# Kernel tuning notes

Hardware: AMD Instinct MI355X
Metric: run time of the kernel (lower is better)

The kernel has to match this reference:

```python
import jax, jax.numpy as jnp
import numpy as np

OS = 14            # output_size
GRID = 2           # ceil(roi_size/OS) = ceil(28/14) = 2 (boxes are built 28x28, sampling_ratio=-1)
NODES = OS * OS    # 196 graph nodes
EPS = 1e-5         # BatchNorm eps
K, B, C, H, W = 256, 4, 256, 112, 112


def _bn_relu(x, g, b, m, v):
    # eval-mode BatchNorm2d followed by ReLU (bn_act_conv prefix)
    s = jax.lax.rsqrt(v + EPS)
    xn = (x - m[None, :, None, None]) * s[None, :, None, None]
    return jax.nn.relu(xn * g[None, :, None, None] + b[None, :, None, None])


def _conv(x, w, b, pad):
    y = jax.lax.conv_general_dilated(x, w, (1, 1), [(pad, pad), (pad, pad)],
                                     dimension_numbers=('NCHW', 'OIHW', 'NCHW'))
    return y + b[None, :, None, None]


def _roi_align(sem, boxes):
    # torchvision roi_align, spatial_scale=1.0, aligned=False, sampling_ratio=-1 (static grid=2)
    Bs, Cc, Hh, Ww = sem.shape
    bidx = boxes[:, 0].astype(jnp.int32)
    x1, y1, x2, y2 = boxes[:, 1], boxes[:, 2], boxes[:, 3], boxes[:, 4]
    bw = jnp.maximum(x2 - x1, 1.0) / OS
    bh = jnp.maximum(y2 - y1, 1.0) / OS
    t = (jnp.arange(OS * GRID, dtype=sem.dtype) + 0.5) / GRID   # pw*GRID+ix collapsed
    xs = x1[:, None] + bw[:, None] * t                          # [K, 28]
    ys = y1[:, None] + bh[:, None] * t

    def prep(c, L):
        m = (c >= -1.0) & (c <= L)
        cc = jnp.clip(c, 0.0, L - 1)
        lo = jnp.floor(cc).astype(jnp.int32)
        hi = jnp.minimum(lo + 1, L - 1)
        return m, lo, hi, cc - lo

    my, yl, yh, ly = prep(ys, Hh)
    mx, xl, xh, lx = prep(xs, Ww)
    semt = jnp.transpose(sem, (0, 2, 3, 1))  # [B,H,W,C]

    def gat(ya, xa):
        return semt[bidx[:, None, None], ya[:, :, None], xa[:, None, :]]  # [K,28,28,C]

    ly_ = ly[:, :, None, None]
    lx_ = lx[:, None, :, None]
    val = (gat(yl, xl) * (1 - ly_) * (1 - lx_) + gat(yl, xh) * (1 - ly_) * lx_
           + gat(yh, xl) * ly_ * (1 - lx_) + gat(yh, xh) * ly_ * lx_)
    val = jnp.where((my[:, :, None] & mx[:, None, :])[..., None], val, 0.0)
    val = val.reshape(-1, OS, GRID, OS, GRID, Cc).mean(axis=(2, 4))  # avg over sampling grid
    return jnp.transpose(val, (0, 3, 1, 2))  # [K,C,14,14]


def _gcn_agg(A, x):
    # PyG gcn_norm on a fully-connected weighted graph (self loops already present):
    # deg[j] = sum_i A[i,j] (scatter on col); out[j] = sum_i d^-1/2[i] A[i,j] d^-1/2[j] x[i]
    deg = A.sum(axis=1)                 # [K,196]
    dis = jax.lax.rsqrt(deg)            # sigmoid weights > 0 => no zero degree
    Nrm = dis[:, :, None] * A * dis[:, None, :]
    return jnp.einsum('kij,kif->kjf', Nrm, x)


def _forward(roi_feature, semantic, boxes,
             bn_sem_g, bn_sem_b, bn_sem_m, bn_sem_v, conv_sem_w, conv_sem_b,
             bn_fpn_g, bn_fpn_b, bn_fpn_m, bn_fpn_v, conv_fpn_w, conv_fpn_b,
             bn_aff_g, bn_aff_b, bn_aff_m, bn_aff_v, conv_aff_w, conv_aff_b,
             gcn1_w, gcn1_b, gcn2_w, gcn2_b):
    roi_sem = _roi_align(semantic, boxes)                                   # [K,256,14,14]
    a = (_conv(_bn_relu(roi_sem, bn_sem_g, bn_sem_b, bn_sem_m, bn_sem_v), conv_sem_w, conv_sem_b, 1)
         + _conv(_bn_relu(roi_feature, bn_fpn_g, bn_fpn_b, bn_fpn_m, bn_fpn_v), conv_fpn_w, conv_fpn_b, 1))
    aff = _conv(_bn_relu(a, bn_aff_g, bn_aff_b, bn_aff_m, bn_aff_v), conv_aff_w, conv_aff_b, 0)
    A = jax.nn.sigmoid(aff.reshape(-1, NODES, NODES))                       # [K,196,196]
    X = roi_feature.reshape(-1, C, NODES).transpose(0, 2, 1)                # [K,196,256] node feats
    x1 = jax.nn.relu(_gcn_agg(A, X @ gcn1_w) + gcn1_b)                      # GCNConv(256,16)+ReLU
    x2 = _gcn_agg(A, x1 @ gcn2_w) + gcn2_b                                  # GCNConv(16,256)
    emb = x2.transpose(0, 2, 1).reshape(-1, C, OS, OS)
    return roi_sem + emb


def setup_inputs() -> dict:
    key = jax.random.key(0)
    ks = jax.random.split(key, 24)
    roi_feature = jax.random.normal(ks[0], (K, C, OS, OS), jnp.float32)
    semantic = jax.random.normal(ks[1], (B, C, H, W), jnp.float32)
    bidx = jax.random.randint(ks[2], (K,), 0, B).astype(jnp.float32)
    xy = jax.random.uniform(ks[3], (K, 2), jnp.float32, 0.0, float(H - 28))
    boxes = jnp.concatenate([bidx[:, None], xy, xy + 28.0], axis=1)  # (idx,x1,y1,x2,y2), 28x28 boxes

    def bn(kg, c):
        k1, k2, k3, k4 = jax.random.split(kg, 4)
        return (jax.random.normal(k1, (c,)) * 0.1 + 1.0,
                jax.random.normal(k2, (c,)) * 0.1,
                jax.random.normal(k3, (c,)) * 0.1,
                jax.random.uniform(k4, (c,), jnp.float32, 0.5, 1.5))
    bn_sem = bn(ks[4], C); bn_fpn = bn(ks[5], C); bn_aff = bn(ks[6], 64)
    inp = {
        'roi_feature': roi_feature, 'semantic': semantic, 'boxes': boxes,
        'bn_sem_g': bn_sem[0], 'bn_sem_b': bn_sem[1], 'bn_sem_m': bn_sem[2], 'bn_sem_v': bn_sem[3],
        'conv_sem_w': jax.random.normal(ks[7], (64, C, 3, 3)) * 0.02,
        'conv_sem_b': jax.random.normal(ks[8], (64,)) * 0.02,
        'bn_fpn_g': bn_fpn[0], 'bn_fpn_b': bn_fpn[1], 'bn_fpn_m': bn_fpn[2], 'bn_fpn_v': bn_fpn[3],
        'conv_fpn_w': jax.random.normal(ks[9], (64, C, 3, 3)) * 0.02,
        'conv_fpn_b': jax.random.normal(ks[10], (64,)) * 0.02,
        'bn_aff_g': bn_aff[0], 'bn_aff_b': bn_aff[1], 'bn_aff_m': bn_aff[2], 'bn_aff_v': bn_aff[3],
        'conv_aff_w': jax.random.normal(ks[11], (NODES, 64, 1, 1)) * 0.05,
        'conv_aff_b': jax.random.normal(ks[12], (NODES,)) * 0.05,
        'gcn1_w': jax.random.normal(ks[13], (C, 16)) * 0.05,
        'gcn1_b': jax.random.normal(ks[14], (16,)) * 0.05,
        'gcn2_w': jax.random.normal(ks[15], (16, C)) * 0.05,
        'gcn2_b': jax.random.normal(ks[16], (C,)) * 0.05,
    }
    return inp


def reference(roi_feature, semantic, boxes,
              bn_sem_g, bn_sem_b, bn_sem_m, bn_sem_v, conv_sem_w, conv_sem_b,
              bn_fpn_g, bn_fpn_b, bn_fpn_m, bn_fpn_v, conv_fpn_w, conv_fpn_b,
              bn_aff_g, bn_aff_b, bn_aff_m, bn_aff_v, conv_aff_w, conv_aff_b,
              gcn1_w, gcn1_b, gcn2_w, gcn2_b):
    return _forward(roi_feature, semantic, boxes,
                    bn_sem_g, bn_sem_b, bn_sem_m, bn_sem_v, conv_sem_w, conv_sem_b,
                    bn_fpn_g, bn_fpn_b, bn_fpn_m, bn_fpn_v, conv_fpn_w, conv_fpn_b,
                    bn_aff_g, bn_aff_b, bn_aff_m, bn_aff_v, conv_aff_w, conv_aff_b,
                    gcn1_w, gcn1_b, gcn2_w, gcn2_b)
```

## Files before the change

### kernel.cpp

```cpp
#include <hip/hip_runtime.h>
#include <hip/hip_bf16.h>

#define KBOX 256
#define CCH  256
#define NODES 196
#define OS 14

typedef __attribute__((ext_vector_type(8))) short  bf16x8;
typedef __attribute__((ext_vector_type(8))) unsigned short u16x8;
typedef __attribute__((ext_vector_type(4))) float  f32x4;
typedef __attribute__((ext_vector_type(4))) short  s16x4;
typedef __attribute__((ext_vector_type(4))) int    i32x4;

__device__ __forceinline__ short f2bf(float x) {
  __hip_bfloat16 h = __float2bfloat16(x);
  return *reinterpret_cast<short*>(&h);
}
__device__ __forceinline__ float bf2f(unsigned short u) {
  unsigned int x = ((unsigned int)u) << 16;
  union { unsigned int i; float f; } c; c.i = x;
  return c.f;
}

#define MFMA16 __builtin_amdgcn_mfma_f32_16x16x32_bf16

__global__ __launch_bounds__(256) void prep_kernel(
    const float* __restrict__ bn_sem_g, const float* __restrict__ bn_sem_b,
    const float* __restrict__ bn_sem_m, const float* __restrict__ bn_sem_v,
    const float* __restrict__ conv_sem_w, const float* __restrict__ conv_sem_b,
    const float* __restrict__ bn_fpn_g, const float* __restrict__ bn_fpn_b,
    const float* __restrict__ bn_fpn_m, const float* __restrict__ bn_fpn_v,
    const float* __restrict__ conv_fpn_w, const float* __restrict__ conv_fpn_b,
    const float* __restrict__ bn_aff_g, const float* __restrict__ bn_aff_b,
    const float* __restrict__ bn_aff_m, const float* __restrict__ bn_aff_v,
    const float* __restrict__ conv_aff_w, const float* __restrict__ g1w,
    const float* __restrict__ g2w,
    float* __restrict__ ss_sem, float* __restrict__ ss_fpn, float* __restrict__ ss_aff2,
    short* __restrict__ wfrag, short* __restrict__ wafrag, short* __restrict__ g1wf,
    short* __restrict__ g2wf)
{
  int gid = blockIdx.x * blockDim.x + threadIdx.x;
  int gsz = gridDim.x * blockDim.x;
  for (int c = gid; c < 256; c += gsz) {
    float s = bn_sem_g[c] * rsqrtf(bn_sem_v[c] + 1e-5f);
    ss_sem[c] = s; ss_sem[256 + c] = bn_sem_b[c] - bn_sem_m[c] * s;
    float s2 = bn_fpn_g[c] * rsqrtf(bn_fpn_v[c] + 1e-5f);
    ss_fpn[c] = s2; ss_fpn[256 + c] = bn_fpn_b[c] - bn_fpn_m[c] * s2;
  }
  for (int c = gid; c < 64; c += gsz) {
    float s = bn_aff_g[c] * rsqrtf(bn_aff_v[c] + 1e-5f);
    float sh = bn_aff_b[c] - bn_aff_m[c] * s;
    float bias = conv_sem_b[c] + conv_fpn_b[c];
    ss_aff2[c] = s; ss_aff2[64 + c] = bias * s + sh;
  }
  for (int idx = gid; idx < 144 * 4 * 64 * 8; idx += gsz) {
    int e = idx & 7, lane = (idx >> 3) & 63, nt = (idx >> 9) & 3, kstep = idx >> 11;
    int src = kstep / 72, rem = kstep % 72, icc = rem / 9, pos = rem % 9;
    int ky = pos / 3, kx = pos % 3;
    int oc = nt * 16 + (lane & 15);
    int ic = icc * 32 + (lane >> 4) * 8 + e;
    const float* w = src ? conv_fpn_w : conv_sem_w;
    wfrag[idx] = f2bf(w[((oc * 256 + ic) * 3 + ky) * 3 + kx]);
  }
  for (int idx = gid; idx < 2 * 13 * 64 * 8; idx += gsz) {
    int t = idx;
    int e = t & 7; t >>= 3;
    int lane = t & 63; t >>= 6;
    int nt = t % 13; int s = t / 13;
    int i = nt * 16 + (lane & 15);
    int ic = s * 32 + (lane >> 4) * 8 + e;
    wafrag[idx] = f2bf(i < NODES ? conv_aff_w[i * 64 + ic] : 0.f);
  }
  for (int idx = gid; idx < 8 * 64 * 8; idx += gsz) {
    int e = idx & 7, lane = (idx >> 3) & 63, ks = idx >> 9;
    int ic = ks * 32 + (lane >> 4) * 8 + e;
    int f = lane & 15;
    g1wf[idx] = f2bf(g1w[ic * 16 + f]);
  }
  for (int idx = gid; idx < 16 * 64 * 8; idx += gsz) {
    int e = idx & 7, lane = (idx >> 3) & 63, ct = idx >> 9;
    int kk = (lane >> 4) * 8 + e;
    int c = ct * 16 + (lane & 15);
    g2wf[idx] = f2bf(kk < 16 ? g2w[kk * 256 + c] : 0.f);
  }
}

__global__ __launch_bounds__(256) void transpose_bf16_kernel(
    const float* __restrict__ in, unsigned short* __restrict__ out, int C, int HW)
{
  __shared__ float tile[64][65];
  int nh = (HW + 63) >> 6;
  int bi = blockIdx.x;
  int cb = bi % (C >> 6); bi /= (C >> 6);
  int hb = bi % nh; int b = bi / nh;
  int tx = threadIdx.x & 63, ty = threadIdx.x >> 6;
  const float* inb = in + (size_t)b * C * HW;
  unsigned short* outb = out + (size_t)b * HW * C;
  #pragma unroll
  for (int i = ty; i < 64; i += 4) {
    int c = cb * 64 + i, hw = hb * 64 + tx;
    tile[i][tx] = (hw < HW) ? inb[(size_t)c * HW + hw] : 0.f;
  }
  __syncthreads();
  int cp = threadIdx.x & 31;
  #pragma unroll
  for (int i = (int)(threadIdx.x >> 5); i < 64; i += 8) {
    int hw = hb * 64 + i;
    if (hw < HW) {
      ushort2 v;
      v.x = (unsigned short)f2bf(tile[cp * 2][i]);
      v.y = (unsigned short)f2bf(tile[cp * 2 + 1][i]);
      *(ushort2*)&outb[(size_t)hw * C + cb * 64 + cp * 2] = v;
    }
  }
}

__global__ __launch_bounds__(512) void roi_align_kernel(
    const unsigned short* __restrict__ semt, const float* __restrict__ boxes,
    unsigned short* __restrict__ roi_sem)
{
  __shared__ unsigned short slab[5][29][256];
  int kb = blockIdx.x / 7, g = blockIdx.x % 7;
  int tid = threadIdx.x, wave = tid >> 6, lane = tid & 63;
  const float* bx = boxes + kb * 5;
  int bb = (int)bx[0];
  float x1 = bx[1], y1 = bx[2];
  float xb = x1 + 0.5f, yv = y1 + 0.5f;
  int X0 = (int)floorf(xb); float fx = xb - (float)X0;
  int Y0 = (int)floorf(yv); float fy = yv - (float)Y0;
  const unsigned short* base = semt + (size_t)bb * 12544 * 256;
  #pragma unroll
  for (int i = 0; i < 19; ++i) {
    int s = wave + i * 8;
    if (s < 145) {
      int r = s / 29, xi = s - r * 29;
      int yr = min(Y0 + 4 * g + r, 111);
      int xc = min(X0 + xi, 111);
      *(s16x4*)&slab[r][xi][lane * 4] =
          *(const s16x4*)(base + ((size_t)yr * 112 + xc) * 256 + lane * 4);
    }
  }
  __syncthreads();
  int c2 = tid & 127, grp = tid >> 7;
  int oyl = grp >> 1, og = grp & 1;
  int rb = oyl * 2;
  float w0 = 1.f - fy;
  unsigned short* op = roi_sem + (((size_t)kb * NODES) + (2 * g + oyl) * OS) * 256 + c2 * 2;
  #pragma unroll
  for (int oxs = 0; oxs < 7; ++oxs) {
    int ox = og * 7 + oxs;
    float o0 = 0.f, o1 = 0.f;
    #pragma unroll
    for (int xi = 0; xi < 3; ++xi) {
      float xw = (xi == 0) ? (1.f - fx) : (xi == 1 ? 1.f : fx);
      const unsigned short* p0 = &slab[rb][2 * ox + xi][c2 * 2];
      const unsigned short* p1 = &slab[rb + 1][2 * ox + xi][c2 * 2];
      const unsigned short* p2 = &slab[rb + 2][2 * ox + xi][c2 * 2];
      o0 += xw * (w0 * bf2f(p0[0]) + bf2f(p1[0]) + fy * bf2f(p2[0]));
      o1 += xw * (w0 * bf2f(p0[1]) + bf2f(p1[1]) + fy * bf2f(p2[1]));
    }
    ushort2 v;
    v.x = (unsigned short)f2bf(o0 * 0.25f);
    v.y = (unsigned short)f2bf(o1 * 0.25f);
    *(ushort2*)(op + (size_t)ox * 256) = v;
  }
}

__global__ __launch_bounds__(256) void conv_ab_kernel(
    const unsigned short* __restrict__ roi_sem, const unsigned short* __restrict__ roif,
    const float* __restrict__ ss_sem, const float* __restrict__ ss_fpn,
    const short* __restrict__ wfrag, const float* __restrict__ ss_aff2,
    short* __restrict__ a_rel)
{
  int k = blockIdx.x;
  int tid = threadIdx.x;
  int wave = tid >> 6, lane = tid & 63;
  int l15 = lane & 15, lq = lane >> 4;
  __shared__ short lds_in[2][197][40];
  __shared__ short lds_wf[2][18432];
  __shared__ float lds_sc[2][256], lds_sh[2][256];
  __shared__ float scA[64], cmbA[64];

  lds_sc[0][tid] = ss_sem[tid]; lds_sh[0][tid] = ss_sem[256 + tid];
  lds_sc[1][tid] = ss_fpn[tid]; lds_sh[1][tid] = ss_fpn[256 + tid];
  if (tid < 64) { scA[tid] = ss_aff2[tid]; cmbA[tid] = ss_aff2[64 + tid]; }
  if (tid < 40) { lds_in[0][196][tid] = 0; lds_in[1][196][tid] = 0; }

  int oyA[4], oxA[4]; bool mvA[4], jvA[4];
  #pragma unroll
  for (int mi = 0; mi < 4; ++mi) {
    int mt = wave + mi * 4;
    mvA[mi] = (mt < 13);
    int j = mt * 16 + l15;
    jvA[mi] = (j < 196);
    int oy = j / 14;
    oyA[mi] = oy; oxA[mi] = j - oy * 14;
  }

  u16x8 inv[4];
  i32x4 wv[9];
  const size_t kbase = (size_t)k * NODES * CCH;

  f32x4 acc[4][4];
  #pragma unroll
  for (int i = 0; i < 4; ++i)
    #pragma unroll
    for (int j = 0; j < 4; ++j) acc[i][j] = f32x4{0.f, 0.f, 0.f, 0.f};

#define ISSUE_LOADS(P) do {                                                  \
    int src_ = (P) >> 3, icc_ = (P) & 7;                                     \
    const unsigned short* in_ = (src_ ? roif : roi_sem) + kbase + icc_ * 32; \
    _Pragma("unroll")                                                        \
    for (int i_ = 0; i_ < 3; ++i_) {                                         \
      int f_ = tid + i_ * 256;                                               \
      inv[i_] = *(const u16x8*)(in_ + (size_t)(f_ >> 2) * 256 + (f_ & 3) * 8); \
    }                                                                        \
    if (tid < 16) {                                                          \
      int f_ = 768 + tid;                                                    \
      inv[3] = *(const u16x8*)(in_ + (size_t)(f_ >> 2) * 256 + (f_ & 3) * 8); \
    }                                                                        \
    const i32x4* wsl_ = (const i32x4*)(wfrag + (size_t)(src_ * 72 + icc_ * 9) * 2048); \
    _Pragma("unroll")                                                        \
    for (int i_ = 0; i_ < 9; ++i_) wv[i_] = wsl_[tid + i_ * 256];            \
  } while (0)

#define WRITE_STAGE(P, BUF) do {                                             \
    int src_ = (P) >> 3, icc_ = (P) & 7;                                     \
    _Pragma("unroll")                                                        \
    for (int i_ = 0; i_ < 3; ++i_) {                                         \
      int f_ = tid + i_ * 256;                                               \
      int j_ = f_ >> 2, cq_ = f_ & 3;                                        \
      bf16x8 pk_;                                                            \
      _Pragma("unroll")                                                      \
      for (int u_ = 0; u_ < 8; ++u_) {                                       \
        int c_ = icc_ * 32 + cq_ * 8 + u_;                                   \
        float x_ = bf2f(inv[i_][u_]) * lds_sc[src_][c_] + lds_sh[src_][c_];  \
        pk_[u_] = f2bf(fmaxf(x_, 0.f));                                      \
      }                                                                      \
      *(bf16x8*)&lds_in[BUF][j_][cq_ * 8] = pk_;                             \
    }                                                                        \
    if (tid < 16) {                                                          \
      int f_ = 768 + tid; int j_ = f_ >> 2, cq_ = f_ & 3;                    \
      bf16x8 pk_;                                                            \
      _Pragma("unroll")                                                      \
      for (int u_ = 0; u_ < 8; ++u_) {                                       \
        int c_ = icc_ * 32 + cq_ * 8 + u_;                                   \
        float x_ = bf2f(inv[3][u_]) * lds_sc[src_][c_] + lds_sh[src_][c_];   \
        pk_[u_] = f2bf(fmaxf(x_, 0.f));                                      \
      }                                                                      \
      *(bf16x8*)&lds_in[BUF][j_][cq_ * 8] = pk_;                             \
    }                                                                        \
    _Pragma("unroll")                                                        \
    for (int i_ = 0; i_ < 9; ++i_) ((i32x4*)lds_wf[BUF])[tid + i_ * 256] = wv[i_]; \
  } while (0)

  ISSUE_LOADS(0);
  __syncthreads();
  WRITE_STAGE(0, 0);
  ISSUE_LOADS(1);
  __syncthreads();

  for (int p = 0; p < 16; ++p) {
    int buf = p & 1;
    if (p < 15) WRITE_STAGE(p + 1, buf ^ 1);
    if (p < 14) ISSUE_LOADS(p + 2);
    #pragma unroll
    for (int pos = 0; pos < 9; ++pos) {
      int ky = pos / 3 - 1, kx = pos % 3 - 1;
      bf16x8 bfr[4];
      #pragma unroll
      for (int n = 0; n < 4; ++n)
        bfr[n] = *(const bf16x8*)&lds_wf[buf][((pos * 4 + n) * 64 + lane) * 8];
      #pragma unroll
      for (int mi = 0; mi < 4; ++mi) {
        if (!mvA[mi]) continue;
        int ny = oyA[mi] + ky, nx = oxA[mi] + kx;
        bool v = jvA[mi] & ((unsigned)ny < 14u) & ((unsigned)nx < 14u);
        int np = v ? (ny * 14 + nx) : 196;
        bf16x8 afr = *(const bf16x8*)&lds_in[buf][np][lq * 8];
        acc[mi][0] = MFMA16(afr, bfr[0], acc[mi][0], 0, 0, 0);
        acc[mi][1] = MFMA16(afr, bfr[1], acc[mi][1], 0, 0, 0);
        acc[mi][2] = MFMA16(afr, bfr[2], acc[mi][2], 0, 0, 0);
        acc[mi][3] = MFMA16(afr, bfr[3], acc[mi][3], 0, 0, 0);
      }
    }
    __syncthreads();
  }

  #pragma unroll
  for (int mi = 0; mi < 4; ++mi) {
    int mt = wave + mi * 4;
    if (mt >= 13) continue;
    #pragma unroll
    for (int n = 0; n < 4; ++n) {
      int oc = n * 16 + l15;
      float sa = scA[oc], cb = cmbA[oc];
      #pragma unroll
      for (int r = 0; r < 4; ++r) {
        int j = mt * 16 + lq * 4 + r;
        if (j < NODES) {
          float t = fmaxf(acc[mi][n][r] * sa + cb, 0.f);
          a_rel[((size_t)k * NODES + j) * 64 + oc] = f2bf(t);
        }
      }
    }
  }
#undef ISSUE_LOADS
#undef WRITE_STAGE
}

__global__ __launch_bounds__(1024, 1) void graph_kernel(
    const short* __restrict__ a_rel, const short* __restrict__ wafrag,
    const float* __restrict__ aff_b, const short* __restrict__ g1wf,
    const float* __restrict__ g1b, const unsigned short* __restrict__ roif_bf,
    const short* __restrict__ g2wf, const float* __restrict__ g2b,
    const unsigned short* __restrict__ roi_sem, float* __restrict__ outp)
{
  __shared__ __align__(16) char smem[125840];
  const int tid = threadIdx.x, wave = tid >> 6, lane = tid & 63;
  const int l15 = lane & 15, lq = lane >> 4;
  const int k = blockIdx.x;

  char*  Ab   = smem;
  short* wa   = (short*)(smem + 96512);
  short* yfr  = (short*)(smem + 96512);
  short* zsf  = (short*)(smem + 103680);
  float* dsl  = (float*)(smem + 123136);
  float* g1bl = (float*)(smem + 123968);
  float* g2bl = (float*)(smem + 124032);
  float* affb = (float*)(smem + 125056);

  const bool wv13 = (wave < 13);
  const int jr  = wave * 16 + l15;
  const int jrc = min(jr, 195);
  const i32x4 z4 = {};

  bf16x8 af0 = {}, af1 = {};
  if (wv13) {
    const short* ap = a_rel + (size_t)k * 12544 + jrc * 64 + lq * 8;
    af0 = *(const bf16x8*)ap;
    af1 = *(const bf16x8*)(ap + 32);
  }
  {
    i32x4 w0 = ((const i32x4*)wafrag)[tid];
    i32x4 w1 = z4;
    if (tid < 640) w1 = ((const i32x4*)wafrag)[1024 + tid];
    if (tid < 832) {
      int r = tid >> 2, q = tid & 3;
      *(i32x4*)(Ab + r * 464 + 384 + q * 16) = z4;
    }
    if (tid < 196) affb[tid] = aff_b[tid];
    if (tid < 256) g2bl[tid] = g2b[tid];
    if (tid < 16)  g1bl[tid] = g1b[tid];
    ((i32x4*)wa)[tid] = w0;
    if (tid < 640) ((i32x4*)wa)[1024 + tid] = w1;
  }
  __syncthreads();

  if (wv13) {
    float rsum[4] = {0.f, 0.f, 0.f, 0.f};
    #pragma unroll
    for (int n = 0; n < 13; ++n) {
      bf16x8 b0 = *(const bf16x8*)(wa + (n * 64 + lane) * 8);
      bf16x8 b1 = *(const bf16x8*)(wa + ((13 + n) * 64 + lane) * 8);
      f32x4 acc = {0.f, 0.f, 0.f, 0.f};
      acc = MFMA16(af0, b0, acc, 0, 0, 0);
      acc = MFMA16(af1, b1, acc, 0, 0, 0);
      int i = n * 16 + l15;
      bool iv = (i < 196);
      float bv = affb[iv ? i : 0];
      #pragma unroll
      for (int r = 0; r < 4; ++r) {
        float v = acc[r] + bv;
        float s = 1.f / (1.f + __expf(-v));
        if (iv) {
          rsum[r] += s;
          *(short*)(Ab + (wave * 16 + lq * 4 + r) * 464 + i * 2) = f2bf(s);
        }
      }
    }
    #pragma unroll
    for (int r = 0; r < 4; ++r) {
      float v = rsum[r];
      v += __shfl_xor(v, 1); v += __shfl_xor(v, 2);
      v += __shfl_xor(v, 4); v += __shfl_xor(v, 8);
      int j = wave * 16 + lq * 4 + r;
      if (l15 == 0 && j < 196) dsl[j] = rsqrtf(v);
    }
  }
  __syncthreads();

  *(i32x4*)(smem + 96512 + tid * 16) = z4;
  if (tid < 256) *(i32x4*)(smem + 96512 + (1024 + tid) * 16) = z4;
  f32x4 xacc = {0.f, 0.f, 0.f, 0.f};
  if (wv13) {
    const unsigned short* Xp = roif_bf + (size_t)k * 50176 + (size_t)jrc * 256 + lq * 8;
    #pragma unroll
    for (int ks = 0; ks < 8; ++ks) {
      bf16x8 xa = *(const bf16x8*)(Xp + ks * 32);
      bf16x8 xb = *(const bf16x8*)(g1wf + (ks * 64 + lane) * 8);
      xacc = MFMA16(xa, xb, xacc, 0, 0, 0);
    }
  }
  __syncthreads();

  if (wv13) {
    #pragma unroll
    for (int r = 0; r < 4; ++r) {
      int i = wave * 16 + lq * 4 + r;
      if (i < 196) {
        float yv = dsl[i] * xacc[r];
        yfr[((i >> 5) * 64 + ((i >> 3) & 3) * 16 + l15) * 8 + (i & 7)] = f2bf(yv);
      }
    }
  }
  __syncthreads();

  f32x4 g0 = {0.f, 0.f, 0.f, 0.f};
  if (wv13) {
    #pragma unroll
    for (int ks = 0; ks < 7; ++ks) {
      bf16x8 bb = *(const bf16x8*)(yfr + (ks * 64 + lane) * 8);
      bf16x8 a0 = *(const bf16x8*)(Ab + jr * 464 + ks * 64 + lq * 16);
      g0 = MFMA16(a0, bb, g0, 0, 0, 0);
    }
  }
  __syncthreads();
  if (wv13) {
    #pragma unroll
    for (int r = 0; r < 4; ++r) {
      int i = wave * 16 + lq * 4 + r;
      if (i < 196) {
        float d = dsl[i];
        float x1v = fmaxf(g0[r] * d + g1bl[l15], 0.f);
        yfr[((i >> 5) * 64 + ((i >> 3) & 3) * 16 + l15) * 8 + (i & 7)] = f2bf(d * x1v);
      }
    }
  }
  __syncthreads();

  if (wv13) {
    f32x4 z0 = {0.f, 0.f, 0.f, 0.f};
    #pragma unroll
    for (int ks = 0; ks < 7; ++ks) {
      bf16x8 bb = *(const bf16x8*)(yfr + (ks * 64 + lane) * 8);
      bf16x8 a0 = *(const bf16x8*)(Ab + jr * 464 + ks * 64 + lq * 16);
      z0 = MFMA16(a0, bb, z0, 0, 0, 0);
    }
    #pragma unroll
    for (int r = 0; r < 4; ++r) {
      int j = wave * 16 + lq * 4 + r;
      if (j < 196) {
        float zv = z0[r] * dsl[j];
        zsf[((j >> 4) * 64 + (l15 >> 3) * 16 + (j & 15)) * 8 + (l15 & 7)] = f2bf(zv);
      }
    }
  }
  __syncthreads();

  {
    bf16x8 wf = *(const bf16x8*)(g2wf + (wave * 64 + lane) * 8);
    const unsigned short* rsmk = roi_sem + (size_t)k * 50176;
    float* op = outp + (size_t)k * 50176;
    float gbv[4];
    #pragma unroll
    for (int r = 0; r < 4; ++r) gbv[r] = g2bl[wave * 16 + lq * 4 + r];
    #pragma unroll
    for (int jt = 0; jt < 13; ++jt) {
      bf16x8 zb = *(const bf16x8*)(zsf + (jt * 64 + lane) * 8);
      f32x4 d = {0.f, 0.f, 0.f, 0.f};
      d = MFMA16(wf, zb, d, 0, 0, 0);
      int j = jt * 16 + l15;
      if (j < 196) {
        #pragma unroll
        for (int r = 0; r < 4; ++r) {
          int c = wave * 16 + lq * 4 + r;
          op[(size_t)c * 196 + j] = d[r] + gbv[r] + bf2f(rsmk[(size_t)j * 256 + c]);
        }
      }
    }
  }
}

extern "C" void kernel_launch(void* const* d_in, const int* in_sizes, int n_in,
                              void* d_out, int out_size, void* d_ws, size_t ws_size,
                              hipStream_t stream) {
  const float* roi_feature = (const float*)d_in[0];
  const float* semantic    = (const float*)d_in[1];
  const float* boxes       = (const float*)d_in[2];
  const float* bn_sem_g = (const float*)d_in[3];
  const float* bn_sem_b = (const float*)d_in[4];
  const float* bn_sem_m = (const float*)d_in[5];
  const float* bn_sem_v = (const float*)d_in[6];
  const float* conv_sem_w = (const float*)d_in[7];
  const float* conv_sem_b = (const float*)d_in[8];
  const float* bn_fpn_g = (const float*)d_in[9];
  const float* bn_fpn_b = (const float*)d_in[10];
  const float* bn_fpn_m = (const float*)d_in[11];
  const float* bn_fpn_v = (const float*)d_in[12];
  const float* conv_fpn_w = (const float*)d_in[13];
  const float* conv_fpn_b = (const float*)d_in[14];
  const float* bn_aff_g = (const float*)d_in[15];
  const float* bn_aff_b = (const float*)d_in[16];
  const float* bn_aff_m = (const float*)d_in[17];
  const float* bn_aff_v = (const float*)d_in[18];
  const float* conv_aff_w = (const float*)d_in[19];
  const float* conv_aff_b = (const float*)d_in[20];
  const float* gcn1_w = (const float*)d_in[21];
  const float* gcn1_b = (const float*)d_in[22];
  const float* gcn2_w = (const float*)d_in[23];
  const float* gcn2_b = (const float*)d_in[24];

  const size_t FT = (size_t)KBOX * NODES * CCH;
  unsigned short* ws16      = (unsigned short*)d_ws;
  unsigned short* semt_bf   = ws16;
  unsigned short* roif_bf   = semt_bf + FT;
  unsigned short* roi_sem_b = roif_bf + FT;
  short*          a_rel     = (short*)(roi_sem_b + FT);
  float*          ss_sem    = (float*)(a_rel + 3211264);
  float*          ss_fpn    = ss_sem + 512;
  float*          ss_aff2   = ss_fpn + 512;
  short*          wfrag     = (short*)(ss_aff2 + 128);
  short*          wafrag    = wfrag + 294912;
  short*          g1wf      = wafrag + 13312;
  short*          g2wf      = g1wf + 4096;

  prep_kernel<<<256, 256, 0, stream>>>(
      bn_sem_g, bn_sem_b, bn_sem_m, bn_sem_v, conv_sem_w, conv_sem_b,
      bn_fpn_g, bn_fpn_b, bn_fpn_m, bn_fpn_v, conv_fpn_w, conv_fpn_b,
      bn_aff_g, bn_aff_b, bn_aff_m, bn_aff_v, conv_aff_w, gcn1_w, gcn2_w,
      ss_sem, ss_fpn, ss_aff2, wfrag, wafrag, g1wf, g2wf);

  transpose_bf16_kernel<<<4 * 196 * 4, 256, 0, stream>>>(semantic, semt_bf, 256, 12544);
  transpose_bf16_kernel<<<4 * 4 * 256, 256, 0, stream>>>(roi_feature, roif_bf, 256, 196);
  roi_align_kernel<<<KBOX * 7, 512, 0, stream>>>(semt_bf, boxes, roi_sem_b);
  conv_ab_kernel<<<KBOX, 256, 0, stream>>>(roi_sem_b, roif_bf, ss_sem, ss_fpn, wfrag, ss_aff2, a_rel);
  graph_kernel<<<KBOX, 1024, 0, stream>>>(a_rel, wafrag, conv_aff_b, g1wf, gcn1_b, roif_bf,
                                          g2wf, gcn2_b, roi_sem_b, (float*)d_out);
}
```

Measured before the change: 161.5 us.

## Split conv over kernel positions across 8 waves with LDS reduction

Rewrites the fused 3x3 conv kernel to use 512 threads. Each wave pair takes a subset of the 9 kernel taps and half the output channels. Each block stages all 256 input channels of one source into LDS at once, padded to a row stride of 268, instead of double-buffering 32-channel slices. Weight fragments are now read straight from global memory rather than through LDS. Partial sums from the tap groups are combined through an LDS reduction before the BN/ReLU epilogue. This adds more parallel waves per block and removes the per-slice pipeline syncs, at the cost of 104 accumulator registers per lane, uneven tap counts across groups, and global weight reads inside the MFMA loop.

```diff
diff --git a/kernel.cpp b/kernel.cpp
--- a/kernel.cpp
+++ b/kernel.cpp
@@ -166,147 +166,160 @@
   }
 }
 
-__global__ __launch_bounds__(256) void conv_ab_kernel(
+__global__ __launch_bounds__(512) void conv_ab_kernel(
     const unsigned short* __restrict__ roi_sem, const unsigned short* __restrict__ roif,
     const float* __restrict__ ss_sem, const float* __restrict__ ss_fpn,
-    const short* __restrict__ wfrag, const float* __restrict__ ss_aff2,
+    const float* __restrict__ ss_aff2, const short* __restrict__ wfrag,
     short* __restrict__ a_rel)
 {
-  int k = blockIdx.x;
-  int tid = threadIdx.x;
-  int wave = tid >> 6, lane = tid & 63;
-  int l15 = lane & 15, lq = lane >> 4;
-  __shared__ short lds_in[2][197][40];
-  __shared__ short lds_wf[2][18432];
-  __shared__ float lds_sc[2][256], lds_sh[2][256];
+  __shared__ short inLDS[198 * 268];
   __shared__ float scA[64], cmbA[64];
-
-  lds_sc[0][tid] = ss_sem[tid]; lds_sh[0][tid] = ss_sem[256 + tid];
-  lds_sc[1][tid] = ss_fpn[tid]; lds_sh[1][tid] = ss_fpn[256 + tid];
+  const int k = blockIdx.x;
+  const int tid = threadIdx.x;
+  const int wave = tid >> 6, lane = tid & 63;
+  const int l15 = lane & 15, lq = lane >> 4;
+  const int pg = wave >> 1, ng = wave & 1;
+  const int p0 = (pg == 0) ? 0 : (pg * 2 + 1);
+  const int p1 = p0 + ((pg == 0) ? 3 : 2);
+
   if (tid < 64) { scA[tid] = ss_aff2[tid]; cmbA[tid] = ss_aff2[64 + tid]; }
-  if (tid < 40) { lds_in[0][196][tid] = 0; lds_in[1][196][tid] = 0; }
-
-  int oyA[4], oxA[4]; bool mvA[4], jvA[4];
+  if (tid < 34) {
+    bf16x8 z = {};
+    *(bf16x8*)&inLDS[196 * 268 + tid * 8] = z;
+  }
+
+  int oyA[13], oxA[13];
   #pragma unroll
-  for (int mi = 0; mi < 4; ++mi) {
-    int mt = wave + mi * 4;
-    mvA[mi] = (mt < 13);
+  for (int mt = 0; mt < 13; ++mt) {
     int j = mt * 16 + l15;
-    jvA[mi] = (j < 196);
     int oy = j / 14;
-    oyA[mi] = oy; oxA[mi] = j - oy * 14;
-  }
-
-  u16x8 inv[4];
-  i32x4 wv[9];
-  const size_t kbase = (size_t)k * NODES * CCH;
-
-  f32x4 acc[4][4];
+    oyA[mt] = oy; oxA[mt] = j - oy * 14;
+  }
+  const int c0 = (tid & 31) * 8;
+
+  f32x4 acc[13][2];
   #pragma unroll
-  for (int i = 0; i < 4; ++i)
-    #pragma unroll
-    for (int j = 0; j < 4; ++j) acc[i][j] = f32x4{0.f, 0.f, 0.f, 0.f};
-
-#define ISSUE_LOADS(P) do {                                                  \
-    int src_ = (P) >> 3, icc_ = (P) & 7;                                     \
-    const unsigned short* in_ = (src_ ? roif : roi_sem) + kbase + icc_ * 32; \
-    _Pragma("unroll")                                                        \
-    for (int i_ = 0; i_ < 3; ++i_) {                                         \
-      int f_ = tid + i_ * 256;                                               \
-      inv[i_] = *(const u16x8*)(in_ + (size_t)(f_ >> 2) * 256 + (f_ & 3) * 8); \
-    }                                                                        \
-    if (tid < 16) {                                                          \
-      int f_ = 768 + tid;                                                    \
-      inv[3] = *(const u16x8*)(in_ + (size_t)(f_ >> 2) * 256 + (f_ & 3) * 8); \
-    }                                                                        \
-    const i32x4* wsl_ = (const i32x4*)(wfrag + (size_t)(src_ * 72 + icc_ * 9) * 2048); \
-    _Pragma("unroll")                                                        \
-    for (int i_ = 0; i_ < 9; ++i_) wv[i_] = wsl_[tid + i_ * 256];            \
-  } while (0)
-
-#define WRITE_STAGE(P, BUF) do {                                             \
-    int src_ = (P) >> 3, icc_ = (P) & 7;                                     \
-    _Pragma("unroll")                                                        \
-    for (int i_ = 0; i_ < 3; ++i_) {                                         \
-      int f_ = tid + i_ * 256;                                               \
-      int j_ = f_ >> 2, cq_ = f_ & 3;                                        \
-      bf16x8 pk_;                                                            \
-      _Pragma("unroll")                                                      \
-      for (int u_ = 0; u_ < 8; ++u_) {                                       \
-        int c_ = icc_ * 32 + cq_ * 8 + u_;                                   \
-        float x_ = bf2f(inv[i_][u_]) * lds_sc[src_][c_] + lds_sh[src_][c_];  \
-        pk_[u_] = f2bf(fmaxf(x_, 0.f));                                      \
-      }                                                                      \
-      *(bf16x8*)&lds_in[BUF][j_][cq_ * 8] = pk_;                             \
-    }                                                                        \
-    if (tid < 16) {                                                          \
-      int f_ = 768 + tid; int j_ = f_ >> 2, cq_ = f_ & 3;                    \
-      bf16x8 pk_;                                                            \
-      _Pragma("unroll")                                                      \
-      for (int u_ = 0; u_ < 8; ++u_) {                                       \
-        int c_ = icc_ * 32 + cq_ * 8 + u_;                                   \
-        float x_ = bf2f(inv[3][u_]) * lds_sc[src_][c_] + lds_sh[src_][c_];   \
-        pk_[u_] = f2bf(fmaxf(x_, 0.f));                                      \
-      }                                                                      \
-      *(bf16x8*)&lds_in[BUF][j_][cq_ * 8] = pk_;                             \
-    }                                                                        \
-    _Pragma("unroll")                                                        \
-    for (int i_ = 0; i_ < 9; ++i_) ((i32x4*)lds_wf[BUF])[tid + i_ * 256] = wv[i_]; \
-  } while (0)
-
-  ISSUE_LOADS(0);
-  __syncthreads();
-  WRITE_STAGE(0, 0);
-  ISSUE_LOADS(1);
-  __syncthreads();
-
-  for (int p = 0; p < 16; ++p) {
-    int buf = p & 1;
-    if (p < 15) WRITE_STAGE(p + 1, buf ^ 1);
-    if (p < 14) ISSUE_LOADS(p + 2);
-    #pragma unroll
-    for (int pos = 0; pos < 9; ++pos) {
+  for (int mt = 0; mt < 13; ++mt) {
+    acc[mt][0] = f32x4{0.f, 0.f, 0.f, 0.f};
+    acc[mt][1] = f32x4{0.f, 0.f, 0.f, 0.f};
+  }
+
+  for (int src = 0; src < 2; ++src) {
+    const unsigned short* inp = (src ? roif : roi_sem) + (size_t)k * NODES * CCH;
+    const float* ss = src ? ss_fpn : ss_sem;
+    f32x4 sc0 = *(const f32x4*)(ss + c0);
+    f32x4 sc1 = *(const f32x4*)(ss + c0 + 4);
+    f32x4 sh0 = *(const f32x4*)(ss + 256 + c0);
+    f32x4 sh1 = *(const f32x4*)(ss + 256 + c0 + 4);
+    __syncthreads();
+    #pragma unroll
+    for (int i = 0; i < 12; ++i) {
+      int j = (tid >> 5) + i * 16;
+      u16x8 v = *(const u16x8*)(inp + (size_t)j * 256 + c0);
+      bf16x8 pk;
+      #pragma unroll
+      for (int u = 0; u < 4; ++u) pk[u] = f2bf(fmaxf(bf2f(v[u]) * sc0[u] + sh0[u], 0.f));
+      #pragma unroll
+      for (int u = 0; u < 4; ++u) pk[4 + u] = f2bf(fmaxf(bf2f(v[4 + u]) * sc1[u] + sh1[u], 0.f));
+      *(bf16x8*)&inLDS[j * 268 + c0] = pk;
+    }
+    if (tid < 128) {
+      int j = 192 + (tid >> 5);
+      u16x8 v = *(const u16x8*)(inp + (size_t)j * 256 + c0);
+      bf16x8 pk;
+      #pragma unroll
+      for (int u = 0; u < 4; ++u) pk[u] = f2bf(fmaxf(bf2f(v[u]) * sc0[u] + sh0[u], 0.f));
+      #pragma unroll
+      for (int u = 0; u < 4; ++u) pk[4 + u] = f2bf(fmaxf(bf2f(v[4 + u]) * sc1[u] + sh1[u], 0.f));
+      *(bf16x8*)&inLDS[j * 268 + c0] = pk;
+    }
+    __syncthreads();
+
+    for (int pos = p0; pos < p1; ++pos) {
       int ky = pos / 3 - 1, kx = pos % 3 - 1;
-      bf16x8 bfr[4];
-      #pragma unroll
-      for (int n = 0; n < 4; ++n)
-        bfr[n] = *(const bf16x8*)&lds_wf[buf][((pos * 4 + n) * 64 + lane) * 8];
-      #pragma unroll
-      for (int mi = 0; mi < 4; ++mi) {
-        if (!mvA[mi]) continue;
-        int ny = oyA[mi] + ky, nx = oxA[mi] + kx;
-        bool v = jvA[mi] & ((unsigned)ny < 14u) & ((unsigned)nx < 14u);
-        int np = v ? (ny * 14 + nx) : 196;
-        bf16x8 afr = *(const bf16x8*)&lds_in[buf][np][lq * 8];
-        acc[mi][0] = MFMA16(afr, bfr[0], acc[mi][0], 0, 0, 0);
-        acc[mi][1] = MFMA16(afr, bfr[1], acc[mi][1], 0, 0, 0);
-        acc[mi][2] = MFMA16(afr, bfr[2], acc[mi][2], 0, 0, 0);
-        acc[mi][3] = MFMA16(afr, bfr[3], acc[mi][3], 0, 0, 0);
-      }
-    }
-    __syncthreads();
-  }
-
-  #pragma unroll
-  for (int mi = 0; mi < 4; ++mi) {
-    int mt = wave + mi * 4;
-    if (mt >= 13) continue;
-    #pragma unroll
-    for (int n = 0; n < 4; ++n) {
-      int oc = n * 16 + l15;
-      float sa = scA[oc], cb = cmbA[oc];
-      #pragma unroll
-      for (int r = 0; r < 4; ++r) {
-        int j = mt * 16 + lq * 4 + r;
-        if (j < NODES) {
-          float t = fmaxf(acc[mi][n][r] * sa + cb, 0.f);
-          a_rel[((size_t)k * NODES + j) * 64 + oc] = f2bf(t);
-        }
-      }
-    }
-  }
-#undef ISSUE_LOADS
-#undef WRITE_STAGE
+      int np[13];
+      #pragma unroll
+      for (int mt = 0; mt < 13; ++mt) {
+        int ny = oyA[mt] + ky, nx = oxA[mt] + kx;
+        bool v = ((unsigned)ny < 14u) & ((unsigned)nx < 14u) & ((mt * 16 + l15) < 196);
+        np[mt] = v ? (ny * 14 + nx) : 196;
+      }
+      #pragma unroll
+      for (int icc = 0; icc < 8; ++icc) {
+        const short* wp = wfrag +
+            ((size_t)((src * 72 + icc * 9 + pos) * 4 + ng * 2) * 64 + lane) * 8;
+        bf16x8 b0 = *(const bf16x8*)wp;
+        bf16x8 b1 = *(const bf16x8*)(wp + 512);
+        #pragma unroll
+        for (int mt = 0; mt < 13; ++mt) {
+          bf16x8 a = *(const bf16x8*)&inLDS[np[mt] * 268 + icc * 32 + lq * 8];
+          acc[mt][0] = MFMA16(a, b0, acc[mt][0], 0, 0, 0);
+          acc[mt][1] = MFMA16(a, b1, acc[mt][1], 0, 0, 0);
+        }
+      }
+    }
+  }
+
+  float* red = (float*)inLDS;
+  __syncthreads();
+  if (pg == 1 || pg == 3) {
+    float* dst = red + (size_t)((pg >> 1) * 2 + ng) * 6272;
+    #pragma unroll
+    for (int mt = 0; mt < 13; ++mt)
+      #pragma unroll
+      for (int nn = 0; nn < 2; ++nn)
+        #pragma unroll
+        for (int r = 0; r < 4; ++r) {
+          int j = mt * 16 + lq * 4 + r;
+          if (j < 196) dst[j * 32 + nn * 16 + l15] = acc[mt][nn][r];
+        }
+  }
+  __syncthreads();
+  if (pg == 0 || pg == 2) {
+    const float* sb = red + (size_t)((pg >> 1) * 2 + ng) * 6272;
+    #pragma unroll
+    for (int mt = 0; mt < 13; ++mt)
+      #pragma unroll
+      for (int nn = 0; nn < 2; ++nn)
+        #pragma unroll
+        for (int r = 0; r < 4; ++r) {
+          int j = mt * 16 + lq * 4 + r;
+          if (j < 196) acc[mt][nn][r] += sb[j * 32 + nn * 16 + l15];
+        }
+  }
+  __syncthreads();
+  if (pg == 2) {
+    float* dst = red + (size_t)ng * 6272;
+    #pragma unroll
+    for (int mt = 0; mt < 13; ++mt)
+      #pragma unroll
+      for (int nn = 0; nn < 2; ++nn)
+        #pragma unroll
+        for (int r = 0; r < 4; ++r) {
+          int j = mt * 16 + lq * 4 + r;
+          if (j < 196) dst[j * 32 + nn * 16 + l15] = acc[mt][nn][r];
+        }
+  }
+  __syncthreads();
+  if (pg == 0) {
+    const float* sb = red + (size_t)ng * 6272;
+    short* op = a_rel + (size_t)k * 12544;
+    #pragma unroll
+    for (int mt = 0; mt < 13; ++mt)
+      #pragma unroll
+      for (int nn = 0; nn < 2; ++nn) {
+        int oc = (ng * 2 + nn) * 16 + l15;
+        float sa = scA[oc], cb = cmbA[oc];
+        #pragma unroll
+        for (int r = 0; r < 4; ++r) {
+          int j = mt * 16 + lq * 4 + r;
+          if (j < 196) {
+            float t = acc[mt][nn][r] + sb[j * 32 + nn * 16 + l15];
+            op[j * 64 + oc] = f2bf(fmaxf(t * sa + cb, 0.f));
+          }
+        }
+      }
+  }
 }
 
 __global__ __launch_bounds__(1024, 1) void graph_kernel(
@@ -534,7 +547,8 @@
   transpose_bf16_kernel<<<4 * 196 * 4, 256, 0, stream>>>(semantic, semt_bf, 256, 12544);
   transpose_bf16_kernel<<<4 * 4 * 256, 256, 0, stream>>>(roi_feature, roif_bf, 256, 196);
   roi_align_kernel<<<KBOX * 7, 512, 0, stream>>>(semt_bf, boxes, roi_sem_b);
-  conv_ab_kernel<<<KBOX, 256, 0, stream>>>(roi_sem_b, roif_bf, ss_sem, ss_fpn, wfrag, ss_aff2, a_rel);
+  conv_ab_kernel<<<KBOX, 512, 0, stream>>>(roi_sem_b, roif_bf, ss_sem, ss_fpn, ss_aff2,
+                                           wfrag, a_rel);
   graph_kernel<<<KBOX, 1024, 0, stream>>>(a_rel, wafrag, conv_aff_b, g1wf, gcn1_b, roif_bf,
                                           g2wf, gcn2_b, roi_sem_b, (float*)d_out);
 }
```

Result: no change. 163.4 us, median of 2 (+1.2%).
